# Kernel tuning notes

Measured on AMD Instinct MI355X. Metric: run time of the kernel, lower is better.

## Reference

```python
import jax, jax.numpy as jnp
import numpy as np

H, D = 4, 32
HID = H * D  # 128
NA, NW, NO = 100_000, 20_000, 50_000
E = 150_000
OFFS = (0, NA, NA + NW, NA + NW + NO)
NTOT = OFFS[3]
# node order: assignments=0, workers=1, orders=2
# edge types (src_type, dst_type): w->a, o->a, a->w, a->o
ETYPES = ((1, 0), (2, 0), (0, 1), (0, 2))


def setup_inputs() -> dict:
    key = jax.random.key(0)
    ks = jax.random.split(key, 20)
    s = 0.05
    return {
        "x_a": jax.random.normal(ks[0], (NA, 64), jnp.float32),
        "x_w": jax.random.normal(ks[1], (NW, 64), jnp.float32),
        "x_o": jax.random.normal(ks[2], (NO, 64), jnp.float32),
        "W_in": jax.random.normal(ks[3], (3, 64, HID), jnp.float32) * s,
        "b_in": jnp.zeros((3, HID), jnp.float32),
        "W_kqv": jax.random.normal(ks[4], (2, 3, HID, 3 * HID), jnp.float32) * s,
        "b_kqv": jnp.zeros((2, 3, 3 * HID), jnp.float32),
        "a_rel": jax.random.normal(ks[5], (2, 4, H, D, D), jnp.float32) * s,
        "m_rel": jax.random.normal(ks[6], (2, 4, H, D, D), jnp.float32) * s,
        "p_rel": jnp.ones((2, 4, H), jnp.float32),
        "skip_p": jnp.ones((2, 3), jnp.float32),
        "W_o": jax.random.normal(ks[7], (2, 3, HID, HID), jnp.float32) * s,
        "b_o": jnp.zeros((2, 3, HID), jnp.float32),
        "ln_g": jnp.ones((2, 3, HID), jnp.float32),
        "ln_b": jnp.zeros((2, 3, HID), jnp.float32),
        "w_head": jax.random.normal(ks[8], (HID, 1), jnp.float32) * s,
        "b_head": jnp.zeros((1,), jnp.float32),
        "base": jnp.zeros((1,), jnp.float32),
        "src_wa": jax.random.randint(ks[9], (E,), 0, NW),
        "dst_wa": jax.random.randint(ks[10], (E,), 0, NA),
        "src_oa": jax.random.randint(ks[11], (E,), 0, NO),
        "dst_oa": jax.random.randint(ks[12], (E,), 0, NA),
        "src_aw": jax.random.randint(ks[13], (E,), 0, NA),
        "dst_aw": jax.random.randint(ks[14], (E,), 0, NW),
        "src_ao": jax.random.randint(ks[15], (E,), 0, NA),
        "dst_ao": jax.random.randint(ks[16], (E,), 0, NO),
    }


def _ln(x, g, b):
    mu = jnp.mean(x, axis=-1, keepdims=True)
    var = jnp.var(x, axis=-1, keepdims=True)
    return (x - mu) * jax.lax.rsqrt(var + 1e-5) * g + b


def _hgt_forward(x_a, x_w, x_o, W_in, b_in, W_kqv, b_kqv, a_rel, m_rel, p_rel,
                 skip_p, W_o, b_o, ln_g, ln_b, w_head, b_head, base, edges):
    # input projection + relu per node type
    xs = [jax.nn.relu(x @ W_in[t] + b_in[t]) for t, x in enumerate((x_a, x_w, x_o))]
    scale = 1.0 / np.sqrt(D).astype(np.float32)
    for l in range(2):  # num_layers (structurally distinct params)
        # per-node-type fused K/Q/V projection (PyG kqv_lin)
        kqv = [xs[t] @ W_kqv[l, t] + b_kqv[l, t] for t in range(3)]
        kd = [m[:, :HID].reshape(-1, H, D) for m in kqv]
        qd = [m[:, HID:2 * HID].reshape(-1, H, D) for m in kqv]
        vd = [m[:, 2 * HID:].reshape(-1, H, D) for m in kqv]
        alphas, vals, dsts = [], [], []
        for e, (st, dt) in enumerate(ETYPES):  # 4 relation types
            src, dst = edges[e]
            # per-edge-type per-head relation transforms applied at node level
            ke = jnp.einsum('nhd,hde->nhe', kd[st], a_rel[l, e])
            ve = jnp.einsum('nhd,hde->nhe', vd[st], m_rel[l, e])
            kg = ke[src]            # [E,H,D] gather
            vg = ve[src]
            qg = qd[dt][dst]
            alphas.append((qg * kg).sum(-1) * p_rel[l, e] * scale)  # [E,H]
            vals.append(vg)
            dsts.append(OFFS[dt] + dst)
        alpha = jnp.concatenate(alphas, axis=0)   # [Etot,H]
        vall = jnp.concatenate(vals, axis=0)      # [Etot,H,D]
        dstg = jnp.concatenate(dsts, axis=0)      # [Etot]
        # segment softmax over all incoming edges of each destination node
        amax = jax.ops.segment_max(alpha, dstg, num_segments=NTOT)
        ex = jnp.exp(alpha - amax[dstg])
        den = jax.ops.segment_sum(ex, dstg, num_segments=NTOT)
        w = ex / (den[dstg] + 1e-16)
        agg = jax.ops.segment_sum(w[:, :, None] * vall, dstg, num_segments=NTOT)
        agg = agg.reshape(NTOT, HID)
        new_xs = []
        for t in range(3):
            o = agg[OFFS[t]:OFFS[t + 1]]
            o = jax.nn.gelu(o, approximate=False) @ W_o[l, t] + b_o[l, t]
            g = jax.nn.sigmoid(skip_p[l, t])
            o = g * o + (1.0 - g) * xs[t]
            new_xs.append(jax.nn.relu(_ln(o, ln_g[l, t], ln_b[l, t])))
        xs = new_xs
    delta = (xs[0] @ w_head)[:, 0] + b_head[0]
    return base[0] + delta  # [NA]


def reference(x_a, x_w, x_o, W_in, b_in, W_kqv, b_kqv, a_rel, m_rel, p_rel,
              skip_p, W_o, b_o, ln_g, ln_b, w_head, b_head, base,
              src_wa, dst_wa, src_oa, dst_oa, src_aw, dst_aw, src_ao, dst_ao):
    edges = ((src_wa, dst_wa), (src_oa, dst_oa), (src_aw, dst_aw), (src_ao, dst_ao))
    return _hgt_forward(x_a, x_w, x_o, W_in, b_in, W_kqv, b_kqv, a_rel, m_rel,
                        p_rel, skip_p, W_o, b_o, ln_g, ln_b, w_head, b_head,
                        base, edges)
```

## Files before the change

kernel.cpp:

```cpp
#include <hip/hip_runtime.h>
#include <cstddef>
#include <cmath>

namespace {

constexpr int H = 4, D = 32, HID = 128;
constexpr int NA = 100000, NW = 20000, NO = 50000;
constexpr int NTOT = NA + NW + NO;
constexpr int E = 150000;
constexpr float SCALE = 0.17677669529663687f;
constexpr int LDK = 3 * HID;

typedef __attribute__((ext_vector_type(8))) short short8v;
typedef __attribute__((ext_vector_type(4))) float f32x4;

__device__ __forceinline__ float gelu_exact(float x) {
  return 0.5f * x * (1.f + erff(x * 0.7071067811865475f));
}
__device__ __forceinline__ unsigned short f2bf(float f) {
  unsigned u = __float_as_uint(f);
  return (unsigned short)((u + 0x7FFF + ((u >> 16) & 1)) >> 16);
}
__device__ __forceinline__ float bf2f(unsigned short s) {
  return __uint_as_float(((unsigned)s) << 16);
}

__device__ __forceinline__ int btype(int bx, int nb0, int nb01) {
  return bx < nb0 ? 0 : (bx < nb01 ? 1 : 2);
}

template <int KSTEPS, bool A_FP32>
__device__ __forceinline__ void gemm_body(
    const void* __restrict__ Av, int lda, const unsigned short* __restrict__ BT,
    int ldb, f32x4* acc, int M, int bm) {
  __shared__ unsigned short As[64 * 64];
  __shared__ unsigned short Bs[128 * 64];
  const int tid = threadIdx.x;
  const int wv = tid >> 6, l = tid & 63;
  for (int ks = 0; ks < KSTEPS; ks++) {
    const int kk = ks * 64;
    #pragma unroll
    for (int p = 0; p < 2; p++) {
      int idx = tid + p * 256;
      int r = idx >> 3, c = idx & 7;
      int gr = bm + r;
      unsigned short tmp[8] = {0, 0, 0, 0, 0, 0, 0, 0};
      if (gr < M) {
        if (A_FP32) {
          const float* src = (const float*)Av + (size_t)gr * lda + kk + c * 8;
          float4 f0 = *(const float4*)src;
          float4 f1 = *(const float4*)(src + 4);
          tmp[0] = f2bf(f0.x); tmp[1] = f2bf(f0.y);
          tmp[2] = f2bf(f0.z); tmp[3] = f2bf(f0.w);
          tmp[4] = f2bf(f1.x); tmp[5] = f2bf(f1.y);
          tmp[6] = f2bf(f1.z); tmp[7] = f2bf(f1.w);
        } else {
          *(uint4*)tmp = *(const uint4*)((const unsigned short*)Av +
                                         (size_t)gr * lda + kk + c * 8);
        }
      }
      *(uint4*)&As[r * 64 + ((c ^ (r & 7)) * 8)] = *(const uint4*)tmp;
    }
    #pragma unroll
    for (int p = 0; p < 4; p++) {
      int idx = tid + p * 256;
      int r = idx >> 3, c = idx & 7;
      uint4 v = *(const uint4*)(BT + (size_t)r * ldb + kk + c * 8);
      *(uint4*)&Bs[r * 64 + ((c ^ (r & 7)) * 8)] = v;
    }
    __syncthreads();
    const int arow = wv * 16 + (l & 15);
    #pragma unroll
    for (int ksub = 0; ksub < 2; ksub++) {
      int ch = ksub * 4 + (l >> 4);
      short8v af = *(const short8v*)&As[arow * 64 + ((ch ^ (arow & 7)) * 8)];
      #pragma unroll
      for (int n = 0; n < 8; n++) {
        int brow = n * 16 + (l & 15);
        short8v bf =
            *(const short8v*)&Bs[brow * 64 + ((ch ^ (brow & 7)) * 8)];
        acc[n] =
            __builtin_amdgcn_mfma_f32_16x16x32_bf16(af, bf, acc[n], 0, 0, 0);
      }
    }
    __syncthreads();
  }
}

__global__ __launch_bounds__(256) void prep_weights(
    const float* __restrict__ W_in, const float* __restrict__ W_kqv,
    const float* __restrict__ W_o, unsigned short* __restrict__ WinT,
    unsigned short* __restrict__ Wk0T, unsigned short* __restrict__ WoT) {
  int idx = blockIdx.x * 256 + threadIdx.x;
  const int N1 = 3 * 128 * 64, N2 = 2 * 384 * 128, N3 = 6 * 128 * 128;
  if (idx < N1) {
    int t = idx / 8192, rem = idx - t * 8192;
    int n = rem >> 6, k = rem & 63;
    WinT[idx] = f2bf(W_in[(size_t)t * 64 * 128 + (size_t)k * 128 + n]);
  } else if (idx < N1 + N2) {
    int r = idx - N1;
    int lyr = r / (384 * 128), rem = r - lyr * (384 * 128);
    int n = rem >> 7, k = rem & 127;
    Wk0T[r] = f2bf(W_kqv[(size_t)lyr * 3 * 128 * 384 + (size_t)k * 384 + n]);
  } else if (idx < N1 + N2 + N3) {
    int r = idx - N1 - N2;
    int lt = r / (128 * 128), rem = r - lt * (128 * 128);
    int n = rem >> 7, k = rem & 127;
    WoT[r] = f2bf(W_o[(size_t)lt * 128 * 128 + (size_t)k * 128 + n]);
  }
}

__global__ __launch_bounds__(256) void fold_weights(
    const float* __restrict__ Wl, const float* __restrict__ bl,
    const float* __restrict__ Al, const float* __restrict__ Ml,
    unsigned short* __restrict__ WeT, float* __restrict__ be) {
  int idx = blockIdx.x * 256 + threadIdx.x;
  const int NW_ = 2 * 128 * 384;
  if (idx < NW_) {
    int tt = idx / (128 * 384);
    int rem = idx - tt * (128 * 384);
    int r = rem / 384, c = rem - r * 384;
    int slice = c >> 7, h = (c >> 5) & 3, j = c & 31;
    const float* Wsrc = Wl + (size_t)(tt + 1) * 128 * 384 + (size_t)r * 384;
    float acc = 0.f;
    if (slice == 0) {
      const float* A = Al + ((size_t)tt * H + h) * D * D;
      for (int d = 0; d < 32; d++) acc += Wsrc[h * 32 + d] * A[d * 32 + j];
    } else if (slice == 1) {
      const float* A = Al + ((size_t)(2 + tt) * H + h) * D * D;
      for (int e = 0; e < 32; e++)
        acc += Wsrc[128 + h * 32 + e] * A[j * 32 + e];
    } else {
      const float* Mm = Ml + ((size_t)tt * H + h) * D * D;
      for (int d = 0; d < 32; d++)
        acc += Wsrc[256 + h * 32 + d] * Mm[d * 32 + j];
    }
    WeT[(size_t)tt * 384 * 128 + (size_t)c * 128 + r] = f2bf(acc);
  } else if (idx < NW_ + 2 * 384) {
    int rem = idx - NW_;
    int tt = rem / 384, c = rem - tt * 384;
    int slice = c >> 7, h = (c >> 5) & 3, j = c & 31;
    const float* bsrc = bl + (size_t)(tt + 1) * 384;
    float acc = 0.f;
    if (slice == 0) {
      const float* A = Al + ((size_t)tt * H + h) * D * D;
      for (int d = 0; d < 32; d++) acc += bsrc[h * 32 + d] * A[d * 32 + j];
    } else if (slice == 1) {
      const float* A = Al + ((size_t)(2 + tt) * H + h) * D * D;
      for (int e = 0; e < 32; e++)
        acc += bsrc[128 + h * 32 + e] * A[j * 32 + e];
    } else {
      const float* Mm = Ml + ((size_t)tt * H + h) * D * D;
      for (int d = 0; d < 32; d++)
        acc += bsrc[256 + h * 32 + d] * Mm[d * 32 + j];
    }
    be[rem] = acc;
  }
}

__global__ __launch_bounds__(256) void in_fused(
    const float* __restrict__ xa, const float* __restrict__ xw,
    const float* __restrict__ xo, const unsigned short* __restrict__ WinT,
    const float* __restrict__ b_in, unsigned short* __restrict__ xs, int nb0,
    int nb01) {
  int t = btype(blockIdx.x, nb0, nb01);
  int base = t == 0 ? 0 : (t == 1 ? nb0 : nb01);
  int M = t == 0 ? NA : (t == 1 ? NW : NO);
  int off = t == 0 ? 0 : (t == 1 ? NA : NA + NW);
  const float* A = t == 0 ? xa : (t == 1 ? xw : xo);
  const int bm = (blockIdx.x - base) * 64;
  f32x4 acc[8] = {};
  gemm_body<1, true>(A, 64, WinT + (size_t)t * 128 * 64, 64, acc, M, bm);
  const int l = threadIdx.x & 63, wv = threadIdx.x >> 6;
  const float* bias = b_in + t * HID;
  unsigned short* C = xs + (size_t)off * HID;
  #pragma unroll
  for (int n = 0; n < 8; n++) {
    int col = n * 16 + (l & 15);
    float bb = bias[col];
    #pragma unroll
    for (int j = 0; j < 4; j++) {
      int row = bm + wv * 16 + (l >> 4) * 4 + j;
      if (row < M) C[(size_t)row * HID + col] = f2bf(fmaxf(acc[n][j] + bb, 0.f));
    }
  }
}

__global__ __launch_bounds__(256) void kqv_fused(
    const unsigned short* __restrict__ xs, const unsigned short* __restrict__ Wk0Tl,
    const float* __restrict__ b0, const unsigned short* __restrict__ WeT,
    const float* __restrict__ be, unsigned short* __restrict__ kqvB, int nb0,
    int nb01) {
  int t = btype(blockIdx.x, nb0, nb01);
  int base = t == 0 ? 0 : (t == 1 ? nb0 : nb01);
  int M = t == 0 ? NA : (t == 1 ? NW : NO);
  int off = t == 0 ? 0 : (t == 1 ? NA : NA + NW);
  const unsigned short* BT =
      (t == 0 ? Wk0Tl : WeT + (size_t)(t - 1) * 384 * 128);
  const float* bias = t == 0 ? b0 : be + (size_t)(t - 1) * 384;
  const int bm = (blockIdx.x - base) * 64;
  const int bn = blockIdx.y * 128;
  f32x4 acc[8] = {};
  gemm_body<2, false>(xs + (size_t)off * HID, HID, BT + (size_t)bn * 128, 128,
                      acc, M, bm);
  const int l = threadIdx.x & 63, wv = threadIdx.x >> 6;
  unsigned short* C = kqvB + (size_t)off * LDK;
  #pragma unroll
  for (int n = 0; n < 8; n++) {
    int col = bn + n * 16 + (l & 15);
    float bb = bias[col];
    #pragma unroll
    for (int j = 0; j < 4; j++) {
      int row = bm + wv * 16 + (l >> 4) * 4 + j;
      if (row < M) C[(size_t)row * LDK + col] = f2bf(acc[n][j] + bb);
    }
  }
}

__global__ __launch_bounds__(256) void wo_ln_fused(
    const unsigned short* __restrict__ kqvB, const unsigned short* __restrict__ WoTl,
    const float* __restrict__ bl, unsigned short* __restrict__ xs,
    const float* __restrict__ skipl, const float* __restrict__ gll,
    const float* __restrict__ bll, int nb0, int nb01) {
  int t = btype(blockIdx.x, nb0, nb01);
  int base = t == 0 ? 0 : (t == 1 ? nb0 : nb01);
  int M = t == 0 ? NA : (t == 1 ? NW : NO);
  int off = t == 0 ? 0 : (t == 1 ? NA : NA + NW);
  const int bm = (blockIdx.x - base) * 64;
  f32x4 acc[8] = {};
  gemm_body<2, false>(kqvB + (size_t)off * LDK + HID, LDK,
                      WoTl + (size_t)t * 128 * 128, 128, acc, M, bm);
  const int l = threadIdx.x & 63, wv = threadIdx.x >> 6;
  const float* bias = bl + t * HID;
  const float* gln = gll + t * HID;
  const float* bln = bll + t * HID;
  unsigned short* xsT = xs + (size_t)off * HID;
  const float g = 1.f / (1.f + expf(-skipl[t]));
  float bb[8], gl8[8], bl8[8];
  #pragma unroll
  for (int n = 0; n < 8; n++) {
    int col = n * 16 + (l & 15);
    bb[n] = bias[col];
    gl8[n] = gln[col];
    bl8[n] = bln[col];
  }
  #pragma unroll
  for (int j = 0; j < 4; j++) {
    int row = bm + wv * 16 + (l >> 4) * 4 + j;
    bool ok = row < M;
    float vv[8], sum = 0.f, sq = 0.f;
    #pragma unroll
    for (int n = 0; n < 8; n++) {
      int col = n * 16 + (l & 15);
      float xo = ok ? bf2f(xsT[(size_t)row * HID + col]) : 0.f;
      float val = g * (acc[n][j] + bb[n]) + (1.f - g) * xo;
      vv[n] = val;
      sum += val;
      sq += val * val;
    }
    #pragma unroll
    for (int m = 1; m < 16; m <<= 1) {
      sum += __shfl_xor(sum, m, 64);
      sq += __shfl_xor(sq, m, 64);
    }
    float mu = sum * (1.f / 128.f);
    float var = sq * (1.f / 128.f) - mu * mu;
    float r = rsqrtf(var + 1e-5f);
    if (ok) {
      #pragma unroll
      for (int n = 0; n < 8; n++) {
        float y = fmaxf((vv[n] - mu) * r * gl8[n] + bl8[n], 0.f);
        xsT[(size_t)row * HID + n * 16 + (l & 15)] = f2bf(y);
      }
    }
  }
}

__global__ __launch_bounds__(256) void csr_hist4(
    const int* __restrict__ d0, const int* __restrict__ d1,
    const int* __restrict__ d2, const int* __restrict__ d3,
    int* __restrict__ cnt) {
  int t = blockIdx.x * 256 + threadIdx.x;
  if (t >= 4 * E) return;
  int et = t / E, e = t - et * E;
  const int* dp = et == 0 ? d0 : et == 1 ? d1 : et == 2 ? d2 : d3;
  int base = et == 0 ? 0 : et == 1 ? NA : et == 2 ? 2 * NA : 2 * NA + NW;
  atomicAdd(&cnt[base + dp[e]], 1);
}

__global__ __launch_bounds__(256) void scan_block(const int* __restrict__ cnt,
                                                  int* __restrict__ excl,
                                                  int* __restrict__ bsum,
                                                  int n) {
  __shared__ int tmp[256];
  int i = blockIdx.x * 256 + threadIdx.x;
  int v = (i < n) ? cnt[i] : 0;
  tmp[threadIdx.x] = v;
  __syncthreads();
  int acc = v;
  for (int off = 1; off < 256; off <<= 1) {
    int other = (threadIdx.x >= off) ? tmp[threadIdx.x - off] : 0;
    __syncthreads();
    acc += other;
    tmp[threadIdx.x] = acc;
    __syncthreads();
  }
  if (i < n) excl[i] = acc - v;
  if (threadIdx.x == 255) bsum[blockIdx.x] = acc;
}

__global__ __launch_bounds__(256) void scan_bsums(int* __restrict__ bsum,
                                                  int nb) {
  __shared__ int tmp[256];
  __shared__ int carry;
  if (threadIdx.x == 0) carry = 0;
  __syncthreads();
  for (int start = 0; start < nb; start += 256) {
    int i = start + threadIdx.x;
    int v = (i < nb) ? bsum[i] : 0;
    tmp[threadIdx.x] = v;
    __syncthreads();
    int acc = v;
    for (int off = 1; off < 256; off <<= 1) {
      int other = (threadIdx.x >= off) ? tmp[threadIdx.x - off] : 0;
      __syncthreads();
      acc += other;
      tmp[threadIdx.x] = acc;
      __syncthreads();
    }
    int c = carry;
    if (i < nb) bsum[i] = c + acc - v;
    __syncthreads();
    if (threadIdx.x == 255) carry = c + acc;
    __syncthreads();
  }
}

__device__ __forceinline__ void et_of_node(int i, int& et, int& base, int& nd,
                                           int& rpo) {
  if (i < NA) { et = 0; base = 0; nd = NA; rpo = 0; }
  else if (i < 2 * NA) { et = 1; base = NA; nd = NA; rpo = NA + 1; }
  else if (i < 2 * NA + NW) { et = 2; base = 2 * NA; nd = NW; rpo = 2 * (NA + 1); }
  else { et = 3; base = 2 * NA + NW; nd = NO; rpo = 2 * (NA + 1) + NW + 1; }
}

__global__ __launch_bounds__(256) void csr_finalize4(
    int* __restrict__ rpAll, const int* __restrict__ bsum,
    int* __restrict__ cursor) {
  int i = blockIdx.x * 256 + threadIdx.x;
  if (i >= 2 * NA + NW + NO) return;
  int et, base, nd, rpo;
  et_of_node(i, et, base, nd, rpo);
  int local = i - base;
  int v = rpAll[rpo + local] + bsum[et * 512 + (local >> 8)];
  rpAll[rpo + local] = v;
  cursor[base + local] = v;
  if (local == 0) rpAll[rpo + nd] = E;
}

__global__ __launch_bounds__(256) void csr_scatter4(
    const int* __restrict__ d0, const int* __restrict__ d1,
    const int* __restrict__ d2, const int* __restrict__ d3,
    int* __restrict__ cursor, int* __restrict__ ceAll) {
  int t = blockIdx.x * 256 + threadIdx.x;
  if (t >= 4 * E) return;
  int et = t / E, e = t - et * E;
  const int* dp = et == 0 ? d0 : et == 1 ? d1 : et == 2 ? d2 : d3;
  int base = et == 0 ? 0 : et == 1 ? NA : et == 2 ? 2 * NA : 2 * NA + NW;
  int slot = atomicAdd(&cursor[base + dp[e]], 1);
  ceAll[(size_t)et * E + slot] = e;
}

__global__ __launch_bounds__(256) void csr_sort4(const int* __restrict__ rpAll,
                                                 int* __restrict__ ceAll) {
  int i = blockIdx.x * 256 + threadIdx.x;
  if (i >= 2 * NA + NW + NO) return;
  int et, base, nd, rpo;
  et_of_node(i, et, base, nd, rpo);
  int local = i - base;
  int b = rpAll[rpo + local], e = rpAll[rpo + local + 1];
  int* ce = ceAll + (size_t)et * E;
  for (int k = b + 1; k < e; k++) {
    int key = ce[k];
    int j = k - 1;
    while (j >= b && ce[j] > key) { ce[j + 1] = ce[j]; j--; }
    ce[j + 1] = key;
  }
}

__global__ __launch_bounds__(256) void build_sd(
    const int* __restrict__ ce, const int* __restrict__ s0,
    const int* __restrict__ s1, const int* __restrict__ s2,
    const int* __restrict__ s3, int* __restrict__ srcOf) {
  int t = blockIdx.x * 256 + threadIdx.x;
  if (t >= 4 * E) return;
  int et = t / E;
  int e = ce[t];
  const int* sp = et == 0 ? s0 : et == 1 ? s1 : et == 2 ? s2 : s3;
  int sOff = et == 0 ? NA : et == 1 ? NA + NW : 0;
  srcOf[t] = sOff + sp[e];
}

__global__ __launch_bounds__(256) void attn_fused(
    const unsigned short* __restrict__ kqv, const int* __restrict__ rpAll,
    const int* __restrict__ srcOf, const float* __restrict__ Pl,
    const float* __restrict__ Ml, unsigned short* __restrict__ out) {
  int dl = (blockIdx.x * 256 + threadIdx.x) >> 6;
  int lane = threadIdx.x & 63;
  if (dl >= NTOT) return;
  int q = lane >> 4, p = lane & 15;
  int b0, e0, b1 = 0, e1 = 0, et23 = -1;
  const int* so0;
  const int* so1 = srcOf;
  float ps0, ps1 = 0.f;
  if (dl < NA) {
    b0 = rpAll[dl]; e0 = rpAll[dl + 1];
    b1 = rpAll[(NA + 1) + dl]; e1 = rpAll[(NA + 1) + dl + 1];
    so0 = srcOf; so1 = srcOf + E;
    ps0 = Pl[q] * SCALE; ps1 = Pl[H + q] * SCALE;
  } else if (dl < NA + NW) {
    int x = dl - NA;
    b0 = rpAll[2 * (NA + 1) + x]; e0 = rpAll[2 * (NA + 1) + x + 1];
    so0 = srcOf + 2 * (size_t)E;
    ps0 = Pl[2 * H + q] * SCALE;
    et23 = 2;
  } else {
    int x = dl - NA - NW;
    b0 = rpAll[2 * (NA + 1) + (NW + 1) + x];
    e0 = rpAll[2 * (NA + 1) + (NW + 1) + x + 1];
    so0 = srcOf + 3 * (size_t)E;
    ps0 = Pl[3 * H + q] * SCALE;
    et23 = 3;
  }
  const int n0 = e0 - b0;
  const int n01 = n0 + (e1 - b1);
  unsigned qv = *(const unsigned*)(kqv + (size_t)dl * LDK + HID + lane * 2);
  float qx = bf2f((unsigned short)(qv & 0xFFFF));
  float qy = bf2f((unsigned short)(qv >> 16));
  float m = -INFINITY, den = 0.f, ax = 0.f, ay = 0.f;
  for (int t = 0; t < n01; t++) {
    int slot = t < n0 ? b0 + t : b1 + (t - n0);
    const int* so = t < n0 ? so0 : so1;
    float ps = t < n0 ? ps0 : ps1;
    int src = so[slot];
    const unsigned short* row = kqv + (size_t)src * LDK;
    unsigned kv2 = *(const unsigned*)(row + lane * 2);
    unsigned vv = *(const unsigned*)(row + 2 * HID + lane * 2);
    float s = qx * bf2f((unsigned short)(kv2 & 0xFFFF)) +
              qy * bf2f((unsigned short)(kv2 >> 16));
    s += __shfl_xor(s, 1, 64);
    s += __shfl_xor(s, 2, 64);
    s += __shfl_xor(s, 4, 64);
    s += __shfl_xor(s, 8, 64);
    s *= ps;
    float nm = fmaxf(m, s);
    float c = expf(m - nm);
    float w = expf(s - nm);
    den = den * c + w;
    ax = ax * c + w * bf2f((unsigned short)(vv & 0xFFFF));
    ay = ay * c + w * bf2f((unsigned short)(vv >> 16));
    m = nm;
  }
  float inv = 1.f / (den + 1e-16f);
  ax *= inv;
  ay *= inv;
  if (et23 >= 0) {
    const float* Mm = Ml + ((size_t)et23 * H + q) * D * D;
    int base = lane & 48;
    float o0 = 0.f, o1 = 0.f;
    #pragma unroll
    for (int j = 0; j < 16; j++) {
      float s0 = __shfl(ax, base + j, 64);
      float s1 = __shfl(ay, base + j, 64);
      float2 m0 = *(const float2*)&Mm[(2 * j) * 32 + 2 * p];
      float2 m1 = *(const float2*)&Mm[(2 * j + 1) * 32 + 2 * p];
      o0 += s0 * m0.x + s1 * m1.x;
      o1 += s0 * m0.y + s1 * m1.y;
    }
    ax = o0; ay = o1;
  }
  unsigned ov = (unsigned)f2bf(gelu_exact(ax)) |
                ((unsigned)f2bf(gelu_exact(ay)) << 16);
  *(unsigned*)(out + (size_t)dl * LDK + HID + lane * 2) = ov;
}

__global__ __launch_bounds__(256) void head_kernel(
    const unsigned short* __restrict__ xs0, const float* __restrict__ w_head,
    const float* __restrict__ b_head, const float* __restrict__ basep,
    float* __restrict__ out, int Nrows) {
  int wid = (blockIdx.x * 256 + threadIdx.x) >> 6;
  int lane = threadIdx.x & 63;
  if (wid >= Nrows) return;
  size_t base = (size_t)wid * HID;
  float d = bf2f(xs0[base + lane]) * w_head[lane] +
            bf2f(xs0[base + 64 + lane]) * w_head[64 + lane];
  #pragma unroll
  for (int m = 1; m < 64; m <<= 1) d += __shfl_xor(d, m, 64);
  if (lane == 0) out[wid] = basep[0] + b_head[0] + d;
}

}

extern "C" void kernel_launch(void* const* d_in, const int* in_sizes, int n_in,
                              void* d_out, int out_size, void* d_ws,
                              size_t ws_size, hipStream_t stream) {
  const float* x_a = (const float*)d_in[0];
  const float* x_w = (const float*)d_in[1];
  const float* x_o = (const float*)d_in[2];
  const float* W_in = (const float*)d_in[3];
  const float* b_in = (const float*)d_in[4];
  const float* W_kqv = (const float*)d_in[5];
  const float* b_kqv = (const float*)d_in[6];
  const float* a_rel = (const float*)d_in[7];
  const float* m_rel = (const float*)d_in[8];
  const float* p_rel = (const float*)d_in[9];
  const float* skip_p = (const float*)d_in[10];
  const float* W_o = (const float*)d_in[11];
  const float* b_o = (const float*)d_in[12];
  const float* ln_g = (const float*)d_in[13];
  const float* ln_b = (const float*)d_in[14];
  const float* w_head = (const float*)d_in[15];
  const float* b_head = (const float*)d_in[16];
  const float* basep = (const float*)d_in[17];
  const int* srcs[4] = {(const int*)d_in[18], (const int*)d_in[20],
                        (const int*)d_in[22], (const int*)d_in[24]};
  const int* dsts[4] = {(const int*)d_in[19], (const int*)d_in[21],
                        (const int*)d_in[23], (const int*)d_in[25]};

  const size_t SZ_XS = (size_t)NTOT * HID * 2;
  const size_t SZ_KQV = (size_t)NTOT * LDK * 2;
  const size_t SZ_WINT = (size_t)3 * 128 * 64 * 2;
  const size_t SZ_WK0T = (size_t)2 * 384 * 128 * 2;
  const size_t SZ_WOT = (size_t)6 * 128 * 128 * 2;
  const size_t SZ_WET = (size_t)2 * 384 * 128 * 2;
  const size_t SZ_BE = ((size_t)2 * 384 * 4 + 63) & ~63ull;
  const size_t SZ_SD = (size_t)4 * E * 4;
  const int CNT_TOT = 2 * NA + NW + NO;
  const int RP_TOT = 2 * (NA + 1) + (NW + 1) + (NO + 1);
  const size_t SZ_RP = ((size_t)RP_TOT * 4 + 63) & ~63ull;
  const size_t SZ_CE = (size_t)4 * E * 4;
  const size_t SZ_CU = ((size_t)CNT_TOT * 4 + 63) & ~63ull;
  const size_t SZ_BS = 4 * 512 * 4;
  const size_t need = SZ_XS + SZ_KQV + SZ_WINT + SZ_WK0T + SZ_WOT + SZ_WET +
                      SZ_BE + SZ_SD + SZ_RP + SZ_CE + 2 * SZ_CU + SZ_BS;
  if (ws_size < need) return;

  char* p = (char*)d_ws;
  unsigned short* xs = (unsigned short*)p;    p += SZ_XS;
  unsigned short* kqvB = (unsigned short*)p;  p += SZ_KQV;
  unsigned short* WinT = (unsigned short*)p;  p += SZ_WINT;
  unsigned short* Wk0T = (unsigned short*)p;  p += SZ_WK0T;
  unsigned short* WoT = (unsigned short*)p;   p += SZ_WOT;
  unsigned short* WeT = (unsigned short*)p;   p += SZ_WET;
  float* beB = (float*)p;                     p += SZ_BE;
  int* srcOf = (int*)p;                       p += SZ_SD;
  int* rpAll = (int*)p;                       p += SZ_RP;
  int* ceAll = (int*)p;                       p += SZ_CE;
  int* cursor = (int*)p;                      p += SZ_CU;
  int* cnt = (int*)p;                         p += SZ_CU;
  int* bsum = (int*)p;

  const int rpOff[4] = {0, NA + 1, 2 * (NA + 1), 2 * (NA + 1) + NW + 1};
  const int cntBase[4] = {0, NA, 2 * NA, 2 * NA + NW};
  const int ndE[4] = {NA, NA, NW, NO};
  const int e4b = (4 * E + 255) / 256;
  const int nb0 = (NA + 63) / 64, nb01 = nb0 + (NW + 63) / 64;
  const int nbTot = nb01 + (NO + 63) / 64;

  hipMemsetAsync(cnt, 0, (size_t)CNT_TOT * 4, stream);
  csr_hist4<<<e4b, 256, 0, stream>>>(dsts[0], dsts[1], dsts[2], dsts[3], cnt);
  for (int et = 0; et < 4; et++) {
    int nb = (ndE[et] + 255) / 256;
    scan_block<<<nb, 256, 0, stream>>>(cnt + cntBase[et], rpAll + rpOff[et],
                                       bsum + et * 512, ndE[et]);
    scan_bsums<<<1, 256, 0, stream>>>(bsum + et * 512, nb);
  }
  csr_finalize4<<<(CNT_TOT + 255) / 256, 256, 0, stream>>>(rpAll, bsum, cursor);
  csr_scatter4<<<e4b, 256, 0, stream>>>(dsts[0], dsts[1], dsts[2], dsts[3],
                                        cursor, ceAll);
  csr_sort4<<<(CNT_TOT + 255) / 256, 256, 0, stream>>>(rpAll, ceAll);
  build_sd<<<e4b, 256, 0, stream>>>(ceAll, srcs[0], srcs[1], srcs[2], srcs[3],
                                    srcOf);

  prep_weights<<<(3 * 128 * 64 + 2 * 384 * 128 + 6 * 128 * 128 + 255) / 256,
                 256, 0, stream>>>(W_in, W_kqv, W_o, WinT, Wk0T, WoT);
  in_fused<<<nbTot, 256, 0, stream>>>(x_a, x_w, x_o, WinT, b_in, xs, nb0, nb01);

  const size_t DD = (size_t)H * D * D;
  for (int l = 0; l < 2; l++) {
    const float* Al = a_rel + (size_t)l * 4 * DD;
    const float* Ml = m_rel + (size_t)l * 4 * DD;
    const float* Pl = p_rel + (size_t)l * 4 * H;
    const float* Wl = W_kqv + (size_t)l * 3 * HID * LDK;
    const float* bl = b_kqv + (size_t)l * 3 * LDK;
    fold_weights<<<(2 * 128 * 384 + 2 * 384 + 255) / 256, 256, 0, stream>>>(
        Wl, bl, Al, Ml, WeT, beB);
    kqv_fused<<<dim3(nbTot, 3), 256, 0, stream>>>(
        xs, Wk0T + (size_t)l * 384 * 128, bl, WeT, beB, kqvB, nb0, nb01);
    attn_fused<<<(NTOT + 3) / 4, 256, 0, stream>>>(kqvB, rpAll, srcOf, Pl, Ml,
                                                   kqvB);
    wo_ln_fused<<<nbTot, 256, 0, stream>>>(
        kqvB, WoT + (size_t)l * 3 * 128 * 128, b_o + (size_t)l * 3 * HID, xs,
        skip_p + l * 3, ln_g + (size_t)l * 3 * HID, ln_b + (size_t)l * 3 * HID,
        nb0, nb01);
  }
  head_kernel<<<(NA + 3) / 4, 256, 0, stream>>>(xs, w_head, b_head, basep,
                                                (float*)d_out, NA);
}
```

Baseline: 791.6 us.

## Batch attention edges by eight and merge per-type CSR scan launches

The attention kernel now gathers K/V rows for up to eight edges at once, reduces their scores together, and does one online-softmax rescale per chunk with fast __expf. This exposes more memory-level parallelism and cuts the serial shuffle and exp chain per edge. Separately, the four per-edge-type scan_block/scan_bsums launch pairs are merged into one launch each, which reduces launch overhead. The costs are higher register pressure, wasted lanes in partial chunks, and slightly lower exp precision.

```diff
diff --git a/kernel.cpp b/kernel.cpp
--- a/kernel.cpp
+++ b/kernel.cpp
@@ -23,6 +23,12 @@
 }
 __device__ __forceinline__ float bf2f(unsigned short s) {
   return __uint_as_float(((unsigned)s) << 16);
+}
+__device__ __forceinline__ float blo(unsigned w) {
+  return __uint_as_float(w << 16);
+}
+__device__ __forceinline__ float bhi(unsigned w) {
+  return __uint_as_float(w & 0xFFFF0000u);
 }
 
 __device__ __forceinline__ int btype(int bx, int nb0, int nb01) {
@@ -288,13 +294,25 @@
   atomicAdd(&cnt[base + dp[e]], 1);
 }
 
-__global__ __launch_bounds__(256) void scan_block(const int* __restrict__ cnt,
-                                                  int* __restrict__ excl,
-                                                  int* __restrict__ bsum,
-                                                  int n) {
+__global__ __launch_bounds__(256) void scan_block_all(
+    const int* __restrict__ cnt, int* __restrict__ rpAll,
+    int* __restrict__ bsum) {
+  const int nbA = (NA + 255) / 256, nbW = (NW + 255) / 256,
+            nbO = (NO + 255) / 256;
+  int bx = blockIdx.x;
+  int et, bbase, cbase, rpo, n;
+  if (bx < nbA) { et = 0; bbase = 0; cbase = 0; rpo = 0; n = NA; }
+  else if (bx < 2 * nbA) { et = 1; bbase = nbA; cbase = NA; rpo = NA + 1; n = NA; }
+  else if (bx < 2 * nbA + nbW) {
+    et = 2; bbase = 2 * nbA; cbase = 2 * NA; rpo = 2 * (NA + 1); n = NW;
+  } else {
+    et = 3; bbase = 2 * nbA + nbW; cbase = 2 * NA + NW;
+    rpo = 2 * (NA + 1) + (NW + 1); n = NO;
+  }
+  int lb = bx - bbase;
   __shared__ int tmp[256];
-  int i = blockIdx.x * 256 + threadIdx.x;
-  int v = (i < n) ? cnt[i] : 0;
+  int i = lb * 256 + threadIdx.x;
+  int v = (i < n) ? cnt[cbase + i] : 0;
   tmp[threadIdx.x] = v;
   __syncthreads();
   int acc = v;
@@ -305,19 +323,22 @@
     tmp[threadIdx.x] = acc;
     __syncthreads();
   }
-  if (i < n) excl[i] = acc - v;
-  if (threadIdx.x == 255) bsum[blockIdx.x] = acc;
-}
-
-__global__ __launch_bounds__(256) void scan_bsums(int* __restrict__ bsum,
-                                                  int nb) {
+  if (i < n) rpAll[rpo + i] = acc - v;
+  if (threadIdx.x == 255) bsum[et * 512 + lb] = acc;
+}
+
+__global__ __launch_bounds__(256) void scan_bsums_all(int* __restrict__ bsum) {
+  int et = blockIdx.x;
+  int nb = et < 2 ? (NA + 255) / 256 : (et == 2 ? (NW + 255) / 256
+                                                : (NO + 255) / 256);
+  int* bs = bsum + et * 512;
   __shared__ int tmp[256];
   __shared__ int carry;
   if (threadIdx.x == 0) carry = 0;
   __syncthreads();
   for (int start = 0; start < nb; start += 256) {
     int i = start + threadIdx.x;
-    int v = (i < nb) ? bsum[i] : 0;
+    int v = (i < nb) ? bs[i] : 0;
     tmp[threadIdx.x] = v;
     __syncthreads();
     int acc = v;
@@ -329,7 +350,7 @@
       __syncthreads();
     }
     int c = carry;
-    if (i < nb) bsum[i] = c + acc - v;
+    if (i < nb) bs[i] = c + acc - v;
     __syncthreads();
     if (threadIdx.x == 255) carry = c + acc;
     __syncthreads();
@@ -435,30 +456,54 @@
   const int n0 = e0 - b0;
   const int n01 = n0 + (e1 - b1);
   unsigned qv = *(const unsigned*)(kqv + (size_t)dl * LDK + HID + lane * 2);
-  float qx = bf2f((unsigned short)(qv & 0xFFFF));
-  float qy = bf2f((unsigned short)(qv >> 16));
+  float qx = blo(qv), qy = bhi(qv);
+  const int lo2 = lane * 2;
+
   float m = -INFINITY, den = 0.f, ax = 0.f, ay = 0.f;
-  for (int t = 0; t < n01; t++) {
-    int slot = t < n0 ? b0 + t : b1 + (t - n0);
-    const int* so = t < n0 ? so0 : so1;
-    float ps = t < n0 ? ps0 : ps1;
-    int src = so[slot];
-    const unsigned short* row = kqv + (size_t)src * LDK;
-    unsigned kv2 = *(const unsigned*)(row + lane * 2);
-    unsigned vv = *(const unsigned*)(row + 2 * HID + lane * 2);
-    float s = qx * bf2f((unsigned short)(kv2 & 0xFFFF)) +
-              qy * bf2f((unsigned short)(kv2 >> 16));
-    s += __shfl_xor(s, 1, 64);
-    s += __shfl_xor(s, 2, 64);
-    s += __shfl_xor(s, 4, 64);
-    s += __shfl_xor(s, 8, 64);
-    s *= ps;
-    float nm = fmaxf(m, s);
-    float c = expf(m - nm);
-    float w = expf(s - nm);
-    den = den * c + w;
-    ax = ax * c + w * bf2f((unsigned short)(vv & 0xFFFF));
-    ay = ay * c + w * bf2f((unsigned short)(vv >> 16));
+  for (int c0 = 0; c0 < n01; c0 += 8) {
+    int nn = n01 - c0;
+    if (nn > 8) nn = 8;
+    unsigned kk[8], vv[8];
+    float s[8];
+    #pragma unroll
+    for (int t = 0; t < 8; t++) {
+      kk[t] = 0;
+      vv[t] = 0;
+      if (t < nn) {
+        int g = c0 + t;
+        int src = (g < n0) ? so0[b0 + g] : so1[b1 + (g - n0)];
+        const unsigned short* r = kqv + (size_t)src * LDK;
+        kk[t] = *(const unsigned*)(r + lo2);
+        vv[t] = *(const unsigned*)(r + 2 * HID + lo2);
+      }
+    }
+    #pragma unroll
+    for (int t = 0; t < 8; t++) s[t] = qx * blo(kk[t]) + qy * bhi(kk[t]);
+    #pragma unroll
+    for (int st = 1; st <= 8; st <<= 1) {
+      #pragma unroll
+      for (int t = 0; t < 8; t++) s[t] += __shfl_xor(s[t], st, 64);
+    }
+    #pragma unroll
+    for (int t = 0; t < 8; t++) {
+      int g = c0 + t;
+      s[t] = (t < nn) ? s[t] * ((g < n0) ? ps0 : ps1) : -INFINITY;
+    }
+    float cm = s[0];
+    #pragma unroll
+    for (int t = 1; t < 8; t++) cm = fmaxf(cm, s[t]);
+    float nm = fmaxf(m, cm);
+    float cc = __expf(m - nm);
+    den *= cc;
+    ax *= cc;
+    ay *= cc;
+    #pragma unroll
+    for (int t = 0; t < 8; t++) {
+      float w = __expf(s[t] - nm);
+      den += w;
+      ax += w * blo(vv[t]);
+      ay += w * bhi(vv[t]);
+    }
     m = nm;
   }
   float inv = 1.f / (den + 1e-16f);
@@ -477,7 +522,8 @@
       o0 += s0 * m0.x + s1 * m1.x;
       o1 += s0 * m0.y + s1 * m1.y;
     }
-    ax = o0; ay = o1;
+    ax = o0;
+    ay = o1;
   }
   unsigned ov = (unsigned)f2bf(gelu_exact(ax)) |
                 ((unsigned)f2bf(gelu_exact(ay)) << 16);
@@ -560,25 +606,21 @@
   int* cnt = (int*)p;                         p += SZ_CU;
   int* bsum = (int*)p;
 
-  const int rpOff[4] = {0, NA + 1, 2 * (NA + 1), 2 * (NA + 1) + NW + 1};
-  const int cntBase[4] = {0, NA, 2 * NA, 2 * NA + NW};
-  const int ndE[4] = {NA, NA, NW, NO};
+  const int CNTT = 2 * NA + NW + NO;
   const int e4b = (4 * E + 255) / 256;
   const int nb0 = (NA + 63) / 64, nb01 = nb0 + (NW + 63) / 64;
   const int nbTot = nb01 + (NO + 63) / 64;
-
-  hipMemsetAsync(cnt, 0, (size_t)CNT_TOT * 4, stream);
+  const int nbA = (NA + 255) / 256, nbW = (NW + 255) / 256,
+            nbO = (NO + 255) / 256;
+
+  hipMemsetAsync(cnt, 0, (size_t)CNTT * 4, stream);
   csr_hist4<<<e4b, 256, 0, stream>>>(dsts[0], dsts[1], dsts[2], dsts[3], cnt);
-  for (int et = 0; et < 4; et++) {
-    int nb = (ndE[et] + 255) / 256;
-    scan_block<<<nb, 256, 0, stream>>>(cnt + cntBase[et], rpAll + rpOff[et],
-                                       bsum + et * 512, ndE[et]);
-    scan_bsums<<<1, 256, 0, stream>>>(bsum + et * 512, nb);
-  }
-  csr_finalize4<<<(CNT_TOT + 255) / 256, 256, 0, stream>>>(rpAll, bsum, cursor);
+  scan_block_all<<<2 * nbA + nbW + nbO, 256, 0, stream>>>(cnt, rpAll, bsum);
+  scan_bsums_all<<<4, 256, 0, stream>>>(bsum);
+  csr_finalize4<<<(CNTT + 255) / 256, 256, 0, stream>>>(rpAll, bsum, cursor);
   csr_scatter4<<<e4b, 256, 0, stream>>>(dsts[0], dsts[1], dsts[2], dsts[3],
                                         cursor, ceAll);
-  csr_sort4<<<(CNT_TOT + 255) / 256, 256, 0, stream>>>(rpAll, ceAll);
+  csr_sort4<<<(CNTT + 255) / 256, 256, 0, stream>>>(rpAll, ceAll);
   build_sd<<<e4b, 256, 0, stream>>>(ceAll, srcs[0], srcs[1], srcs[2], srcs[3],
                                     srcOf);
 
```

Result: faster. 768.1 us (-3.0%).
